# Optimization experiments

Hardware: AMD Instinct MI355X
Metric: run time of the kernel (lower is better)

## Reference

```python
import jax, jax.numpy as jnp
import numpy as np

N_HEAD = 16

def setup_inputs() -> dict:
    key = jax.random.key(0)
    k1, k2, k3 = jax.random.split(key, 3)
    B, T, C = 2, 2048, 1024
    x = jax.random.normal(k1, (B, T, C), dtype=jnp.float32)
    W_attn = jax.random.normal(k2, (C, 3 * C), dtype=jnp.float32) * (C ** -0.5)
    b_attn = jnp.zeros((3 * C,), dtype=jnp.float32)
    W_proj = jax.random.normal(k3, (C, C), dtype=jnp.float32) * (C ** -0.5)
    b_proj = jnp.zeros((C,), dtype=jnp.float32)
    return {"x": x, "W_attn": W_attn, "b_attn": b_attn, "W_proj": W_proj, "b_proj": b_proj}

def reference(x, W_attn, b_attn, W_proj, b_proj):
    B, T, C = x.shape
    H = N_HEAD
    D = C // H  # head_dim
    scale = D ** -0.5
    qkv = x @ W_attn + b_attn                       # [B,T,3C]
    q, k, v = jnp.split(qkv, 3, axis=-1)
    # [B,T,C] -> [B,H,T,D]
    q = q.reshape(B, T, H, D).transpose(0, 2, 1, 3)
    k = k.reshape(B, T, H, D).transpose(0, 2, 1, 3)
    v = v.reshape(B, T, H, D).transpose(0, 2, 1, 3)
    att = jnp.einsum('bhqd,bhkd->bhqk', q, k) * scale
    causal = jnp.tril(jnp.ones((T, T), dtype=bool))
    att = jnp.where(causal, att, jnp.float32(-jnp.inf))
    att = jax.nn.softmax(att, axis=-1)
    y = jnp.einsum('bhqk,bhkd->bhqd', att, v)       # [B,H,T,D]
    y = y.transpose(0, 2, 1, 3).reshape(B, T, C)
    return y @ W_proj + b_proj
```

## Files before the change

kernel.cpp:

```cpp
#include <hip/hip_runtime.h>

typedef __bf16 bf16;
typedef __bf16 bf16x4 __attribute__((ext_vector_type(4)));
typedef __bf16 bf16x8 __attribute__((ext_vector_type(8)));
typedef short s16x4 __attribute__((ext_vector_type(4)));
typedef float f32x4 __attribute__((ext_vector_type(4)));
typedef unsigned int u32x4 __attribute__((ext_vector_type(4)));

#define NB 2
#define NT 2048
#define NC 1024
#define NH 16
#define ND 64

#if __has_builtin(__builtin_amdgcn_exp2f)
#define EXP2F(x) __builtin_amdgcn_exp2f(x)
#else
#define EXP2F(x) __expf(0.69314718055994531f * (x))
#endif

#if __has_builtin(__builtin_amdgcn_rcpf)
#define RCPF(x) __builtin_amdgcn_rcpf(x)
#else
#define RCPF(x) (1.0f / (x))
#endif

__device__ __forceinline__ void async16(const void* g, void* l) {
  __builtin_amdgcn_global_load_lds(
      (const __attribute__((address_space(1))) void*)g,
      (__attribute__((address_space(3))) void*)l, 16, 0, 0);
}

__device__ __forceinline__ bf16x8 ld8(const bf16* p) {
  return *reinterpret_cast<const bf16x8*>(p);
}
__device__ __forceinline__ bf16x4 ld4(const bf16* p) {
  return *reinterpret_cast<const bf16x4*>(p);
}

__device__ __forceinline__ f32x4 mfma16(bf16x4 a, bf16x4 b, f32x4 c) {
  s16x4 ai = __builtin_bit_cast(s16x4, a);
  s16x4 bi = __builtin_bit_cast(s16x4, b);
#if __has_builtin(__builtin_amdgcn_mfma_f32_16x16x16bf16_1k)
  return __builtin_amdgcn_mfma_f32_16x16x16bf16_1k(ai, bi, c, 0, 0, 0);
#else
  f32x4 d;
  asm("v_mfma_f32_16x16x16_bf16 %0, %1, %2, %3"
      : "=v"(d) : "v"(ai), "v"(bi), "v"(c));
  return d;
#endif
}

__global__ __launch_bounds__(256) void cvt_bf16(const float* __restrict__ src,
                                                bf16* __restrict__ dst, int n) {
  int i = (blockIdx.x * 256 + threadIdx.x) * 8;
  if (i + 8 <= n) {
    const float4* s = (const float4*)(src + i);
    float4 a = s[0], b = s[1];
    bf16x8 o;
    o[0] = (bf16)a.x; o[1] = (bf16)a.y; o[2] = (bf16)a.z; o[3] = (bf16)a.w;
    o[4] = (bf16)b.x; o[5] = (bf16)b.y; o[6] = (bf16)b.z; o[7] = (bf16)b.w;
    *(bf16x8*)(dst + i) = o;
  }
}

__global__ __launch_bounds__(256) void transpose_cvt2(
    const float* __restrict__ Wa, bf16* __restrict__ Da,
    const float* __restrict__ Wp, bf16* __restrict__ Dp) {
  __shared__ float tile[32][33];
  int bx = blockIdx.x;
  const float* src;
  bf16* dst;
  int Cc;
  if (bx < 96) { src = Wa; dst = Da; Cc = 3072; }
  else         { src = Wp; dst = Dp; Cc = 1024; bx -= 96; }
  int tx = threadIdx.x & 31, ty = threadIdx.x >> 5;
  int r0 = blockIdx.y * 32, c0 = bx * 32;
#pragma unroll
  for (int i = 0; i < 4; ++i)
    tile[ty + i * 8][tx] = src[(size_t)(r0 + ty + i * 8) * Cc + c0 + tx];
  __syncthreads();
#pragma unroll
  for (int i = 0; i < 4; ++i)
    dst[(size_t)(c0 + ty + i * 8) * 1024 + r0 + tx] = (bf16)tile[tx][ty + i * 8];
}

__global__ __launch_bounds__(256, 2) void gemm_qkv(
    const bf16* __restrict__ A,
    const bf16* __restrict__ Bt,
    const float* __restrict__ bias,
    bf16* __restrict__ Qo, bf16* __restrict__ Ko, bf16* __restrict__ Vto) {
  const int K = 1024;
  __shared__ bf16 As[128 * 32];
  __shared__ bf16 Bs[128 * 32];
  const int tid = threadIdx.x;
  const int lane = tid & 63, wv = tid >> 6;
  const int quad = lane >> 4, ln = lane & 15;
  const int m0 = blockIdx.x * 128, n0 = blockIdx.y * 128;
  const int wr = (wv >> 1) * 64, wc = (wv & 1) * 64;
  const int rA = tid >> 2, cA = (tid & 3) * 8;
  f32x4 acc[4][4] = {};

  for (int kt = 0; kt < K / 32; ++kt) {
    const int k0 = kt * 32;
#pragma unroll
    for (int inst = 0; inst < 2; ++inst) {
      async16(A + (size_t)(m0 + inst * 64 + rA) * K + k0 + cA,
              &As[inst * 2048 + wv * 512]);
      async16(Bt + (size_t)(n0 + inst * 64 + rA) * K + k0 + cA,
              &Bs[inst * 2048 + wv * 512]);
    }
    __syncthreads();
    bf16x8 aF[4], bF[4];
#pragma unroll
    for (int i = 0; i < 4; ++i) {
      aF[i] = ld8(&As[(wr + i * 16 + ln) * 32 + quad * 8]);
      bF[i] = ld8(&Bs[(wc + i * 16 + ln) * 32 + quad * 8]);
    }
#pragma unroll
    for (int rb = 0; rb < 4; ++rb)
#pragma unroll
      for (int cb = 0; cb < 4; ++cb)
        acc[rb][cb] = __builtin_amdgcn_mfma_f32_16x16x32_bf16(
            aF[rb], bF[cb], acc[rb][cb], 0, 0, 0);
    __syncthreads();
  }
#pragma unroll
  for (int rb = 0; rb < 4; ++rb) {
#pragma unroll
    for (int cb = 0; cb < 4; ++cb) {
      int gn = n0 + wc + cb * 16 + ln;
      int part = gn >> 10, c = gn & 1023;
      int h = c >> 6, dd = c & 63;
      float bs = bias[gn];
      int gm0 = m0 + wr + rb * 16 + quad * 4;
      int b = gm0 >> 11, t0 = gm0 & 2047;
      if (part == 2) {
        bf16x4 vv;
#pragma unroll
        for (int r = 0; r < 4; ++r) vv[r] = (bf16)(acc[rb][cb][r] + bs);
        *(bf16x4*)(Vto + ((size_t)(b * NH + h) * ND + dd) * NT + t0) = vv;
      } else {
        bf16* dst = part == 0 ? Qo : Ko;
        float sc = part == 0 ? 0.18033688f : 1.0f;
#pragma unroll
        for (int r = 0; r < 4; ++r)
          dst[((size_t)(b * NH + h) * NT + t0 + r) * ND + dd] =
              (bf16)((acc[rb][cb][r] + bs) * sc);
      }
    }
  }
}

__global__ __launch_bounds__(512, 4) void flash_attn_kernel(
    const bf16* __restrict__ Qg, const bf16* __restrict__ Kg,
    const bf16* __restrict__ Vtg, bf16* __restrict__ Yg) {
  __shared__ __align__(16) char smem[2][16384];
  const int tid = threadIdx.x;
  const int lane = tid & 63, wv = tid >> 6;
  const int quad = lane >> 4, ln = lane & 15;
  const int bid = blockIdx.x;
  const int qt = 15 - (bid >> 5);
  const int bh = bid & 31;
  const int bb = bh >> 4, hh = bh & 15;
  const int q0w = qt * 128 + wv * 16;
  const bf16* Qp = Qg + ((size_t)bh * NT + q0w) * ND;
  const bf16* Kbase = Kg + (size_t)bh * NT * ND;
  const bf16* Vtbase = Vtg + (size_t)bh * ND * NT;

  const int sub = lane >> 3, sch = lane & 7;
  const int swz = ln & 7;

  bf16x8 qf[2];
#pragma unroll
  for (int ks = 0; ks < 2; ++ks)
    qf[ks] = ld8(Qp + (size_t)ln * ND + ks * 32 + quad * 8);

  f32x4 oacc[4] = {};
  float li = 0.f;

  const int ktiles = 2 * qt + 2;
  const int cw = 2 * qt + 1 + (wv >> 2);

#define STAGE(KT, P)                                                           \
  {                                                                            \
    const int k0s = (KT) * 64;                                                 \
    char* Kl = smem[P];                                                        \
    char* Vl = smem[P] + 8192;                                                 \
    int row = wv * 8 + sub;                                                    \
    int gch = sch ^ sub;                                                       \
    async16(Kbase + (size_t)(k0s + row) * ND + gch * 8, Kl + wv * 8 * 128);    \
    async16(Vtbase + (size_t)row * NT + k0s + gch * 8, Vl + wv * 8 * 128);     \
  }

  STAGE(0, 0);
  for (int kt = 0; kt < ktiles; ++kt) {
    const int p = kt & 1;
    __syncthreads();
    if (kt + 1 < ktiles) STAGE(kt + 1, p ^ 1);
    if (kt < cw) {
      const char* Kl = smem[p];
      const char* Vl = smem[p] + 8192;
      const int k0 = kt * 64;
      f32x4 sacc[4] = {};
#pragma unroll
      for (int ks = 0; ks < 2; ++ks) {
        bf16x8 kfr[4];
#pragma unroll
        for (int cb = 0; cb < 4; ++cb)
          kfr[cb] = *(const bf16x8*)(Kl + (cb * 16 + ln) * 128 +
                                     (((ks * 4 + quad) ^ swz) * 16));
#pragma unroll
        for (int cb = 0; cb < 4; ++cb)
          sacc[cb] = __builtin_amdgcn_mfma_f32_16x16x32_bf16(
              kfr[cb], qf[ks], sacc[cb], 0, 0, 0);
      }
      if (k0 + 63 > q0w) {
        int qr = q0w + ln;
#pragma unroll
        for (int cb = 0; cb < 4; ++cb)
#pragma unroll
          for (int r = 0; r < 4; ++r) {
            int kc = k0 + cb * 16 + quad * 4 + r;
            if (kc > qr) sacc[cb][r] = -1e30f;
          }
      }
      bf16x4 pf[4];
      float rs = 0.f;
#pragma unroll
      for (int cb = 0; cb < 4; ++cb) {
        bf16x4 pv;
#pragma unroll
        for (int r = 0; r < 4; ++r) {
          float pexp = EXP2F(sacc[cb][r]);
          rs += pexp;
          pv[r] = (bf16)pexp;
        }
        pf[cb] = pv;
      }
      li += rs;
#pragma unroll
      for (int cb = 0; cb < 4; ++cb) {
        bf16x4 vfr[4];
#pragma unroll
        for (int db = 0; db < 4; ++db)
          vfr[db] = *(const bf16x4*)(Vl + (db * 16 + ln) * 128 +
                                     (((cb * 2 + (quad >> 1)) ^ swz) * 16) +
                                     (quad & 1) * 8);
#pragma unroll
        for (int db = 0; db < 4; ++db)
          oacc[db] = mfma16(vfr[db], pf[cb], oacc[db]);
      }
    }
  }
#undef STAGE

  li += __shfl_xor(li, 16);
  li += __shfl_xor(li, 32);

  float inv = RCPF(li);
  int row = q0w + ln;
#pragma unroll
  for (int db = 0; db < 4; ++db) {
    bf16x4 ov;
#pragma unroll
    for (int r = 0; r < 4; ++r) ov[r] = (bf16)(oacc[db][r] * inv);
    *(bf16x4*)(Yg + ((size_t)(bb * NT + row)) * NC + hh * 64 + db * 16 +
               quad * 4) = ov;
  }
}

__global__ __launch_bounds__(256, 2) void gemm_proj(
    const bf16* __restrict__ A,
    const bf16* __restrict__ Bt,
    const float* __restrict__ bias,
    float* __restrict__ out) {
  const int K = 1024;
  __shared__ bf16 As[128 * 32];
  __shared__ bf16 Bs[128 * 32];
  const int tid = threadIdx.x;
  const int lane = tid & 63, wv = tid >> 6;
  const int quad = lane >> 4, ln = lane & 15;
  const int m0 = blockIdx.x * 128, n0 = blockIdx.y * 128;
  const int wr = (wv >> 1) * 64, wc = (wv & 1) * 64;
  const int rA = tid >> 2, cA = (tid & 3) * 8;
  f32x4 acc[4][4] = {};

  for (int kt = 0; kt < K / 32; ++kt) {
    const int k0 = kt * 32;
#pragma unroll
    for (int inst = 0; inst < 2; ++inst) {
      async16(A + (size_t)(m0 + inst * 64 + rA) * K + k0 + cA,
              &As[inst * 2048 + wv * 512]);
      async16(Bt + (size_t)(n0 + inst * 64 + rA) * K + k0 + cA,
              &Bs[inst * 2048 + wv * 512]);
    }
    __syncthreads();
    bf16x8 aF[4], bF[4];
#pragma unroll
    for (int i = 0; i < 4; ++i) {
      aF[i] = ld8(&As[(wr + i * 16 + ln) * 32 + quad * 8]);
      bF[i] = ld8(&Bs[(wc + i * 16 + ln) * 32 + quad * 8]);
    }
#pragma unroll
    for (int rb = 0; rb < 4; ++rb)
#pragma unroll
      for (int cb = 0; cb < 4; ++cb)
        acc[rb][cb] = __builtin_amdgcn_mfma_f32_16x16x32_bf16(
            aF[rb], bF[cb], acc[rb][cb], 0, 0, 0);
    __syncthreads();
  }
#pragma unroll
  for (int rb = 0; rb < 4; ++rb) {
#pragma unroll
    for (int cb = 0; cb < 4; ++cb) {
      int gn = n0 + wc + cb * 16 + ln;
      float bs = bias[gn];
#pragma unroll
      for (int r = 0; r < 4; ++r) {
        int gm = m0 + wr + rb * 16 + quad * 4 + r;
        out[(size_t)gm * 1024 + gn] = acc[rb][cb][r] + bs;
      }
    }
  }
}

extern "C" void kernel_launch(void* const* d_in, const int* in_sizes, int n_in,
                              void* d_out, int out_size, void* d_ws, size_t ws_size,
                              hipStream_t stream) {
  const float* x      = (const float*)d_in[0];
  const float* W_attn = (const float*)d_in[1];
  const float* b_attn = (const float*)d_in[2];
  const float* W_proj = (const float*)d_in[3];
  const float* b_proj = (const float*)d_in[4];
  float* out = (float*)d_out;

  bf16* ws  = (bf16*)d_ws;
  bf16* xb  = ws;
  bf16* Wab = xb + (size_t)4096 * 1024;
  bf16* Wpb = Wab + (size_t)3072 * 1024;
  bf16* Qb  = Wpb + (size_t)1024 * 1024;
  bf16* Kb  = Qb + (size_t)32 * 2048 * 64;
  bf16* Vtb = Kb + (size_t)32 * 2048 * 64;
  bf16* Yb  = xb;

  cvt_bf16<<<2048, 256, 0, stream>>>(x, xb, 4096 * 1024);
  transpose_cvt2<<<dim3(128, 32), 256, 0, stream>>>(W_attn, Wab, W_proj, Wpb);
  gemm_qkv<<<dim3(32, 24), 256, 0, stream>>>(xb, Wab, b_attn, Qb, Kb, Vtb);
  flash_attn_kernel<<<512, 512, 0, stream>>>(Qb, Kb, Vtb, Yb);
  gemm_proj<<<dim3(32, 8), 256, 0, stream>>>(Yb, Wpb, b_proj, out);
}
```

Measured before the change: 175.2 us.

## Fuse prep kernels, raise QKV GEMM occupancy, halve proj GEMM tile width

Merges the x conversion and the weight transpose-convert kernels into one launch, which removes a kernel launch and a pipeline gap. Raises the gemm_qkv launch-bounds occupancy hint from 2 to 3 blocks. Shrinks the output projection tile from 128x128 to 128x64, doubling the grid from 256 to 512 blocks so more CUs have work. The trade-off is less data reuse per block in the projection GEMM, and possible register pressure or spills in gemm_qkv.

```diff
diff --git a/kernel.cpp b/kernel.cpp
--- a/kernel.cpp
+++ b/kernel.cpp
@@ -51,31 +51,30 @@
 #endif
 }
 
-__global__ __launch_bounds__(256) void cvt_bf16(const float* __restrict__ src,
-                                                bf16* __restrict__ dst, int n) {
-  int i = (blockIdx.x * 256 + threadIdx.x) * 8;
-  if (i + 8 <= n) {
-    const float4* s = (const float4*)(src + i);
+__global__ __launch_bounds__(256) void prep(
+    const float* __restrict__ x, bf16* __restrict__ xb,
+    const float* __restrict__ Wa, bf16* __restrict__ Da,
+    const float* __restrict__ Wp, bf16* __restrict__ Dp) {
+  int bx = blockIdx.x;
+  if (bx < 2048) {
+    int i = (bx * 256 + threadIdx.x) * 8;
+    const float4* s = (const float4*)(x + i);
     float4 a = s[0], b = s[1];
     bf16x8 o;
     o[0] = (bf16)a.x; o[1] = (bf16)a.y; o[2] = (bf16)a.z; o[3] = (bf16)a.w;
     o[4] = (bf16)b.x; o[5] = (bf16)b.y; o[6] = (bf16)b.z; o[7] = (bf16)b.w;
-    *(bf16x8*)(dst + i) = o;
-  }
-}
-
-__global__ __launch_bounds__(256) void transpose_cvt2(
-    const float* __restrict__ Wa, bf16* __restrict__ Da,
-    const float* __restrict__ Wp, bf16* __restrict__ Dp) {
+    *(bf16x8*)(xb + i) = o;
+    return;
+  }
   __shared__ float tile[32][33];
-  int bx = blockIdx.x;
+  int idx = bx - 2048;
   const float* src;
   bf16* dst;
-  int Cc;
-  if (bx < 96) { src = Wa; dst = Da; Cc = 3072; }
-  else         { src = Wp; dst = Dp; Cc = 1024; bx -= 96; }
+  int Cc, cb, rb;
+  if (idx < 96 * 32) { src = Wa; dst = Da; Cc = 3072; cb = idx % 96; rb = idx / 96; }
+  else { idx -= 96 * 32; src = Wp; dst = Dp; Cc = 1024; cb = idx % 32; rb = idx / 32; }
   int tx = threadIdx.x & 31, ty = threadIdx.x >> 5;
-  int r0 = blockIdx.y * 32, c0 = bx * 32;
+  int r0 = rb * 32, c0 = cb * 32;
 #pragma unroll
   for (int i = 0; i < 4; ++i)
     tile[ty + i * 8][tx] = src[(size_t)(r0 + ty + i * 8) * Cc + c0 + tx];
@@ -85,7 +84,7 @@
     dst[(size_t)(c0 + ty + i * 8) * 1024 + r0 + tx] = (bf16)tile[tx][ty + i * 8];
 }
 
-__global__ __launch_bounds__(256, 2) void gemm_qkv(
+__global__ __launch_bounds__(256, 3) void gemm_qkv(
     const bf16* __restrict__ A,
     const bf16* __restrict__ Bt,
     const float* __restrict__ bias,
@@ -277,33 +276,32 @@
     float* __restrict__ out) {
   const int K = 1024;
   __shared__ bf16 As[128 * 32];
-  __shared__ bf16 Bs[128 * 32];
+  __shared__ bf16 Bs[64 * 32];
   const int tid = threadIdx.x;
   const int lane = tid & 63, wv = tid >> 6;
   const int quad = lane >> 4, ln = lane & 15;
-  const int m0 = blockIdx.x * 128, n0 = blockIdx.y * 128;
-  const int wr = (wv >> 1) * 64, wc = (wv & 1) * 64;
+  const int m0 = blockIdx.x * 128, n0 = blockIdx.y * 64;
+  const int wr = wv * 32;
   const int rA = tid >> 2, cA = (tid & 3) * 8;
-  f32x4 acc[4][4] = {};
+  f32x4 acc[2][4] = {};
 
   for (int kt = 0; kt < K / 32; ++kt) {
     const int k0 = kt * 32;
 #pragma unroll
-    for (int inst = 0; inst < 2; ++inst) {
+    for (int inst = 0; inst < 2; ++inst)
       async16(A + (size_t)(m0 + inst * 64 + rA) * K + k0 + cA,
               &As[inst * 2048 + wv * 512]);
-      async16(Bt + (size_t)(n0 + inst * 64 + rA) * K + k0 + cA,
-              &Bs[inst * 2048 + wv * 512]);
-    }
-    __syncthreads();
-    bf16x8 aF[4], bF[4];
-#pragma unroll
-    for (int i = 0; i < 4; ++i) {
+    async16(Bt + (size_t)(n0 + rA) * K + k0 + cA, &Bs[wv * 512]);
+    __syncthreads();
+    bf16x8 aF[2], bF[4];
+#pragma unroll
+    for (int i = 0; i < 2; ++i)
       aF[i] = ld8(&As[(wr + i * 16 + ln) * 32 + quad * 8]);
-      bF[i] = ld8(&Bs[(wc + i * 16 + ln) * 32 + quad * 8]);
-    }
-#pragma unroll
-    for (int rb = 0; rb < 4; ++rb)
+#pragma unroll
+    for (int i = 0; i < 4; ++i)
+      bF[i] = ld8(&Bs[(i * 16 + ln) * 32 + quad * 8]);
+#pragma unroll
+    for (int rb = 0; rb < 2; ++rb)
 #pragma unroll
       for (int cb = 0; cb < 4; ++cb)
         acc[rb][cb] = __builtin_amdgcn_mfma_f32_16x16x32_bf16(
@@ -311,10 +309,10 @@
     __syncthreads();
   }
 #pragma unroll
-  for (int rb = 0; rb < 4; ++rb) {
+  for (int rb = 0; rb < 2; ++rb) {
 #pragma unroll
     for (int cb = 0; cb < 4; ++cb) {
-      int gn = n0 + wc + cb * 16 + ln;
+      int gn = n0 + cb * 16 + ln;
       float bs = bias[gn];
 #pragma unroll
       for (int r = 0; r < 4; ++r) {
@@ -344,9 +342,9 @@
   bf16* Vtb = Kb + (size_t)32 * 2048 * 64;
   bf16* Yb  = xb;
 
-  cvt_bf16<<<2048, 256, 0, stream>>>(x, xb, 4096 * 1024);
-  transpose_cvt2<<<dim3(128, 32), 256, 0, stream>>>(W_attn, Wab, W_proj, Wpb);
+  prep<<<2048 + 96 * 32 + 32 * 32, 256, 0, stream>>>(x, xb, W_attn, Wab,
+                                                     W_proj, Wpb);
   gemm_qkv<<<dim3(32, 24), 256, 0, stream>>>(xb, Wab, b_attn, Qb, Kb, Vtb);
   flash_attn_kernel<<<512, 512, 0, stream>>>(Qb, Kb, Vtb, Yb);
-  gemm_proj<<<dim3(32, 8), 256, 0, stream>>>(Yb, Wpb, b_proj, out);
-}
+  gemm_proj<<<dim3(32, 16), 256, 0, stream>>>(Yb, Wpb, b_proj, out);
+}
```

Result: faster. 169.7 us (-3.1%).
